# Kernel tuning notes

Hardware: AMD Instinct MI355X
Metric: run time of the kernel (lower is better)

## Reference

```python
import jax, jax.numpy as jnp
import numpy as np

B, N, M, C, K = 2, 8192, 4096, 64, 16
HID = 256
EPS_BN = 1e-5


def setup_inputs() -> dict:
    key = jax.random.key(0)
    ks = jax.random.split(key, 16)
    def rn(i, shape, scale=1.0):
        return jax.random.normal(ks[i], shape, jnp.float32) * scale
    return {
        "pcl": rn(0, (B, M, 3)),
        "pcl_noise": rn(1, (B, N, 3)),
        "feature": rn(2, (B, M, C)),
        # MLP_CONV (2d 1x1): 6 -> 256 (BN+ReLU) -> C
        "w2a": rn(3, (HID, 6), 0.3), "b2a": rn(4, (HID,), 0.1),
        "g2a": 1.0 + rn(5, (HID,), 0.1), "bt2a": rn(6, (HID,), 0.1),
        "w2b": rn(7, (C, HID), 0.1), "b2b": rn(8, (C,), 0.1),
        # MLP_CONV_1d: 3C -> C (BN+ReLU) -> C
        "w1a": rn(9, (C, 3 * C), 0.1), "b1a": rn(10, (C,), 0.1),
        "g1a": 1.0 + rn(11, (C,), 0.1), "bt1a": rn(12, (C,), 0.1),
        "w1b": rn(13, (C, C), 0.1), "b1b": rn(14, (C,), 0.1),
    }


def _sqdist(x, y):  # [B,n,3],[B,m,3] -> [B,n,m]
    return (jnp.sum(x * x, -1, keepdims=True)
            - 2.0 * jnp.einsum('bnc,bmc->bnm', x, y)
            + jnp.sum(y * y, -1)[:, None, :])


def _gather(x, idx):  # x [B,M,D], idx [B,...] -> [B,...,D]
    return jax.vmap(lambda xb, ib: xb[ib])(x, idx)


def _bn(h, g, b):  # inference BatchNorm: running mean 0, var 1
    return h * (g / jnp.sqrt(1.0 + EPS_BN)) + b


def reference(pcl, pcl_noise, feature, w2a, b2a, g2a, bt2a, w2b, b2b,
              w1a, b1a, g1a, bt1a, w1b, b1b):
    # nearest clean point for each noisy point (knn_points K=1)
    close_idx = jnp.argmin(_sqdist(pcl_noise, pcl), axis=-1)          # [B,N]
    close_point = _gather(pcl, close_idx)                             # [B,N,3]
    # K nearest neighbors of close_point within pcl (dil_knn, d=1)
    _, idx = jax.lax.top_k(-_sqdist(close_point, pcl), K)             # [B,N,K]
    knn_points = _gather(pcl, idx)[:, :, 1:, :]                       # [B,N,K-1,3]
    knn_feat = _gather(feature, idx)[:, :, 1:, :]                     # [B,N,K-1,C]
    close_feat = _gather(feature, close_idx)                          # [B,N,C]

    delta = knn_points - pcl_noise[:, :, None, :]                     # [B,N,K-1,3]
    dst = jnp.linalg.norm(delta, axis=-1)                             # [B,N,K-1]
    e = jnp.exp(-10.0 * dst)
    weight = e / (jnp.sum(e, -1, keepdims=True) + 1e-7)               # [B,N,K-1]

    cp = jnp.broadcast_to(close_point[:, :, None, :], delta.shape)
    delta_points = jnp.concatenate([delta, cp], axis=-1)              # [B,N,K-1,6]

    # MLP_CONV2 (1x1 convs over channel dim)
    h = jnp.einsum('bnkc,oc->bnko', delta_points, w2a) + b2a
    h = jax.nn.relu(_bn(h, g2a, bt2a))
    pf = jnp.einsum('bnkc,oc->bnko', h, w2b) + b2b                    # [B,N,K-1,C]

    point_feature = jnp.einsum('bnk,bnkc->bnc', weight, pf)           # [B,N,C]
    co_feature = jnp.einsum('bnk,bnkc->bnc', weight, knn_feat)        # [B,N,C]
    df = jnp.concatenate([close_feat, co_feature, point_feature], -1)  # [B,N,3C]

    # MLP_CONV_1d
    h1 = jnp.einsum('bnc,oc->bno', df, w1a) + b1a
    h1 = jax.nn.relu(_bn(h1, g1a, bt1a))
    return jnp.einsum('bnc,oc->bno', h1, w1b) + b1b                   # [B,N,C]
```

## Files before the change

### kernel.cpp

```cpp
#include <hip/hip_runtime.h>
#include <float.h>

typedef unsigned short u16;
typedef unsigned int u32;
typedef unsigned char u8;

typedef float f32x4 __attribute__((ext_vector_type(4)));
typedef short bh8   __attribute__((ext_vector_type(8)));

__device__ __forceinline__ float bf(u16 u) { return __uint_as_float(((u32)u) << 16); }
__device__ __forceinline__ u16 f2bf(float v) {
    u32 x = __float_as_uint(v);
    u32 r = x + 0x7fffu + ((x >> 16) & 1u);
    return (u16)(r >> 16);
}
__device__ __forceinline__ int detect_f32(const void* probe) {
    const u16* u = (const u16*)probe;
    u16 v = u[(threadIdx.x & 63) * 2];
    int e = (int)((v >> 7) & 0xFF);
    int moderate = (e >= 100) && (e <= 140);
    return __popcll(__ballot(moderate)) < 48;
}
__device__ __forceinline__ float ldv(int f32, const void* p, int i) {
    return f32 ? ((const float*)p)[i] : bf(((const u16*)p)[i]);
}
__device__ __forceinline__ float dot3(float x0, float x1, float x2,
                                      float y0, float y1, float y2) {
    return __fmaf_rn(x2, y2, __fmaf_rn(x1, y1, __fmul_rn(x0, y0)));
}
__device__ __forceinline__ u32 mkey32(float d) {
    u32 f = __float_as_uint(d);
    return f ^ (u32)((((int)f) >> 31) | 0x80000000);
}
__device__ __forceinline__ bh8 ldb(const void* p) { return *(const bh8*)p; }
__device__ __forceinline__ f32x4 mfma16(bh8 a, bh8 b, f32x4 c) {
    return __builtin_amdgcn_mfma_f32_16x16x32_bf16(a, b, c, 0, 0, 0);
}

__global__ __launch_bounds__(256) void k_pre(const void* __restrict__ probe,
                                             const void* __restrict__ w2b,
                                             const void* __restrict__ w1a,
                                             const void* __restrict__ w1b,
                                             u32* __restrict__ canonb,
                                             const void* __restrict__ pcl,
                                             float4* __restrict__ pcl4) {
    int f32 = detect_f32(probe);
    int bx = blockIdx.x, t = threadIdx.x;
    if (bx < 64) {
        int ix = bx * 256 + t;
        const void* src; int j;
        if (ix < 8192)       { src = w2b; j = ix; }
        else if (ix < 14336) { src = w1a; j = ix - 8192; }
        else                 { src = w1b; j = ix - 14336; }
        u32 out;
        if (f32) {
            const float* f = (const float*)src;
            out = ((u32)f2bf(f[2*j+1]) << 16) | (u32)f2bf(f[2*j]);
        } else {
            const u16* su = (const u16*)src;
            out = ((u32)su[2*j+1] << 16) | (u32)su[2*j];
        }
        canonb[ix] = out;
    } else {
        int i = (bx - 64) * 256 + t;
        float x = ldv(f32, pcl, i*3+0), y = ldv(f32, pcl, i*3+1), z = ldv(f32, pcl, i*3+2);
        float s = __fadd_rn(__fadd_rn(__fmul_rn(x,x), __fmul_rn(y,y)), __fmul_rn(z,z));
        pcl4[i] = make_float4(x, y, z, s);
    }
}

__global__ __launch_bounds__(256) void k_close(const float4* __restrict__ pcl4,
                                               const void* __restrict__ noise,
                                               u16* __restrict__ cidx) {
    __shared__ __align__(16) float4 tile[2048];
    int f32 = detect_f32(noise);
    int t = threadIdx.x, g = t >> 4, s = t & 15;
    int q = blockIdx.x * 16 + g;
    int b = q >> 13;
    const float4* src = pcl4 + ((size_t)b << 12);
    float x0 = ldv(f32, noise, q*3+0), x1 = ldv(f32, noise, q*3+1), x2 = ldv(f32, noise, q*3+2);
    float sx = __fadd_rn(__fadd_rn(__fmul_rn(x0,x0), __fmul_rn(x1,x1)), __fmul_rn(x2,x2));
    float bd = FLT_MAX; int bi = 0;
    for (int ch = 0; ch < 2; ++ch) {
        __syncthreads();
#pragma unroll
        for (int i = 0; i < 8; ++i) { int ix = t + (i << 8); tile[ix] = src[(ch << 11) + ix]; }
        __syncthreads();
        for (int j = 0; j < 128; ++j) {
            int cl = (j << 4) + s;
            float4 p = tile[cl];
            float dot = dot3(x0, x1, x2, p.x, p.y, p.z);
            float d = __fadd_rn(__fsub_rn(sx, __fmul_rn(2.0f, dot)), p.w);
            int c = (ch << 11) + cl;
            if (d < bd) { bd = d; bi = c; }
        }
    }
#pragma unroll
    for (int m = 8; m >= 1; m >>= 1) {
        float od = __shfl_xor(bd, m);
        int   oi = __shfl_xor(bi, m);
        if (od < bd || (od == bd && oi < bi)) { bd = od; bi = oi; }
    }
    if (s == 0) cidx[q] = (u16)(bi & 4095);
}

__global__ __launch_bounds__(256) void k_knnh(const float4* __restrict__ pcl4,
                                              u16* __restrict__ knn) {
    __shared__ u8  bins[4096];
    __shared__ u32 hist[256];
    __shared__ u32 skey[256];
    __shared__ u16 sidx[256];
    __shared__ float rmn[4], rmx[4];
    __shared__ u32 scnt;
    __shared__ int ibst;
    int t = threadIdx.x, lane = t & 63, wv = t >> 6;
    int q = blockIdx.x;
    int b = q >> 12;
    const float4* src = pcl4 + ((size_t)b << 12);
    float4 Q = src[q & 4095];
    float x0 = Q.x, x1 = Q.y, x2 = Q.z, sx = Q.w;
    if (t < 256) hist[t] = 0;
    if (t == 0) scnt = 0;
    {
        float4 p = src[t << 4];
        float dot = dot3(x0, x1, x2, p.x, p.y, p.z);
        float d = __fadd_rn(__fsub_rn(sx, __fmul_rn(2.0f, dot)), p.w);
        float mn = d, mx = d;
#pragma unroll
        for (int m = 32; m >= 1; m >>= 1) {
            mn = fminf(mn, __shfl_xor(mn, m));
            mx = fmaxf(mx, __shfl_xor(mx, m));
        }
        if (lane == 0) { rmn[wv] = mn; rmx[wv] = mx; }
    }
    __syncthreads();
    float dmn = fminf(fminf(rmn[0], rmn[1]), fminf(rmn[2], rmn[3]));
    float dmx = fmaxf(fmaxf(rmx[0], rmx[1]), fmaxf(rmx[2], rmx[3]));
    float sc = 1024.0f / fmaxf(dmx - dmn, 1e-20f);
#pragma unroll 4
    for (int j = 0; j < 16; ++j) {
        int cin = (j << 8) + t;
        float4 p = src[cin];
        float dot = dot3(x0, x1, x2, p.x, p.y, p.z);
        float d = __fadd_rn(__fsub_rn(sx, __fmul_rn(2.0f, dot)), p.w);
        float fb = fminf(fmaxf((d - dmn) * sc, 0.0f), 255.0f);
        int bn = (int)fb;
        bins[cin] = (u8)bn;
        if (bn < 255) atomicAdd(&hist[bn], 1u);
    }
    __syncthreads();
    if (t < 64) {
        u32 c0 = hist[4*lane], c1 = hist[4*lane+1];
        u32 c2 = hist[4*lane+2], c3 = hist[4*lane+3];
        u32 loc = c0 + c1 + c2 + c3;
        u32 x = loc;
#pragma unroll
        for (int off = 1; off < 64; off <<= 1) { u32 v = __shfl_up(x, off); if (lane >= off) x += v; }
        u32 excl = x - loc;
        int cand = 999;
        if (excl + c0 >= 16u) cand = 4*lane;
        else if (excl + c0 + c1 >= 16u) cand = 4*lane + 1;
        else if (excl + c0 + c1 + c2 >= 16u) cand = 4*lane + 2;
        else if (excl + loc >= 16u) cand = 4*lane + 3;
#pragma unroll
        for (int m = 32; m >= 1; m >>= 1) cand = min(cand, __shfl_xor(cand, m));
        if (lane == 0) ibst = cand;
    }
    __syncthreads();
    int bstar = ibst;
#pragma unroll
    for (int j = 0; j < 16; ++j) {
        int cin = (j << 8) + t;
        if ((int)bins[cin] <= bstar) {
            u32 pos = atomicAdd(&scnt, 1u);
            if (pos < 256u) {
                float4 p = src[cin];
                float dot = dot3(x0, x1, x2, p.x, p.y, p.z);
                float d = __fadd_rn(__fsub_rn(sx, __fmul_rn(2.0f, dot)), p.w);
                skey[pos] = mkey32(d);
                sidx[pos] = (u16)cin;
            }
        }
    }
    __syncthreads();
    u32 n = scnt;
    if (n <= 256u) {
        for (u32 e = (u32)t; e < n; e += 256u) {
            u32 k = skey[e]; u32 i = (u32)sidx[e];
            int rank = 0;
            for (u32 j = 0; j < n; ++j) {
                u32 kj = skey[j]; u32 ij = (u32)sidx[j];
                rank += (kj < k) || (kj == k && ij < i);
            }
            if (rank < 16) knn[((size_t)q << 4) + rank] = (u16)i;
        }
    } else if (t < 64) {
        u32 k0=~0u,k1=~0u,k2=~0u,k3=~0u,k4=~0u,k5=~0u,k6=~0u,k7=~0u,
            k8=~0u,k9=~0u,k10=~0u,k11=~0u,k12=~0u,k13=~0u,k14=~0u,k15=~0u;
        u32 i0r=0,i1r=0,i2r=0,i3r=0,i4r=0,i5r=0,i6r=0,i7r=0,
            i8r=0,i9r=0,i10r=0,i11r=0,i12r=0,i13r=0,i14r=0,i15r=0;
        for (int j = 0; j < 64; ++j) {
            int cin = (j << 6) + lane;
            float4 p = src[cin];
            float dot = dot3(x0, x1, x2, p.x, p.y, p.z);
            float d = __fadd_rn(__fsub_rn(sx, __fmul_rn(2.0f, dot)), p.w);
            u32 v = mkey32(d); u32 vi = (u32)cin;
            if (v < k15) {
                { u32 c_=(v<k0); u32 nk=c_?v:k0; u32 nv=c_?k0:v; u32 ni=c_?vi:i0r; u32 nj=c_?i0r:vi; k0=nk;i0r=ni;v=nv;vi=nj; }
                { u32 c_=(v<k1); u32 nk=c_?v:k1; u32 nv=c_?k1:v; u32 ni=c_?vi:i1r; u32 nj=c_?i1r:vi; k1=nk;i1r=ni;v=nv;vi=nj; }
                { u32 c_=(v<k2); u32 nk=c_?v:k2; u32 nv=c_?k2:v; u32 ni=c_?vi:i2r; u32 nj=c_?i2r:vi; k2=nk;i2r=ni;v=nv;vi=nj; }
                { u32 c_=(v<k3); u32 nk=c_?v:k3; u32 nv=c_?k3:v; u32 ni=c_?vi:i3r; u32 nj=c_?i3r:vi; k3=nk;i3r=ni;v=nv;vi=nj; }
                { u32 c_=(v<k4); u32 nk=c_?v:k4; u32 nv=c_?k4:v; u32 ni=c_?vi:i4r; u32 nj=c_?i4r:vi; k4=nk;i4r=ni;v=nv;vi=nj; }
                { u32 c_=(v<k5); u32 nk=c_?v:k5; u32 nv=c_?k5:v; u32 ni=c_?vi:i5r; u32 nj=c_?i5r:vi; k5=nk;i5r=ni;v=nv;vi=nj; }
                { u32 c_=(v<k6); u32 nk=c_?v:k6; u32 nv=c_?k6:v; u32 ni=c_?vi:i6r; u32 nj=c_?i6r:vi; k6=nk;i6r=ni;v=nv;vi=nj; }
                { u32 c_=(v<k7); u32 nk=c_?v:k7; u32 nv=c_?k7:v; u32 ni=c_?vi:i7r; u32 nj=c_?i7r:vi; k7=nk;i7r=ni;v=nv;vi=nj; }
                { u32 c_=(v<k8); u32 nk=c_?v:k8; u32 nv=c_?k8:v; u32 ni=c_?vi:i8r; u32 nj=c_?i8r:vi; k8=nk;i8r=ni;v=nv;vi=nj; }
                { u32 c_=(v<k9); u32 nk=c_?v:k9; u32 nv=c_?k9:v; u32 ni=c_?vi:i9r; u32 nj=c_?i9r:vi; k9=nk;i9r=ni;v=nv;vi=nj; }
                { u32 c_=(v<k10); u32 nk=c_?v:k10; u32 nv=c_?k10:v; u32 ni=c_?vi:i10r; u32 nj=c_?i10r:vi; k10=nk;i10r=ni;v=nv;vi=nj; }
                { u32 c_=(v<k11); u32 nk=c_?v:k11; u32 nv=c_?k11:v; u32 ni=c_?vi:i11r; u32 nj=c_?i11r:vi; k11=nk;i11r=ni;v=nv;vi=nj; }
                { u32 c_=(v<k12); u32 nk=c_?v:k12; u32 nv=c_?k12:v; u32 ni=c_?vi:i12r; u32 nj=c_?i12r:vi; k12=nk;i12r=ni;v=nv;vi=nj; }
                { u32 c_=(v<k13); u32 nk=c_?v:k13; u32 nv=c_?k13:v; u32 ni=c_?vi:i13r; u32 nj=c_?i13r:vi; k13=nk;i13r=ni;v=nv;vi=nj; }
                { u32 c_=(v<k14); u32 nk=c_?v:k14; u32 nv=c_?k14:v; u32 ni=c_?vi:i14r; u32 nj=c_?i14r:vi; k14=nk;i14r=ni;v=nv;vi=nj; }
                { u32 c_=(v<k15); u32 nk=c_?v:k15; u32 nv=c_?k15:v; u32 ni=c_?vi:i15r; u32 nj=c_?i15r:vi; k15=nk;i15r=ni;v=nv;vi=nj; }
            }
        }
        u32 myres = 0;
        for (int o = 0; o < 16; ++o) {
            u32 bk = k0, bi2 = i0r;
#pragma unroll
            for (int m = 32; m >= 1; m >>= 1) {
                u32 ok = __shfl_xor(bk, m), oi = __shfl_xor(bi2, m);
                if (ok < bk || (ok == bk && oi < bi2)) { bk = ok; bi2 = oi; }
            }
            if (lane == o) myres = bi2;
            if (k0 == bk && i0r == bi2) {
                k0=k1; i0r=i1r; k1=k2; i1r=i2r; k2=k3; i2r=i3r; k3=k4; i3r=i4r;
                k4=k5; i4r=i5r; k5=k6; i5r=i6r; k6=k7; i6r=i7r; k7=k8; i7r=i8r;
                k8=k9; i8r=i9r; k9=k10; i9r=i10r; k10=k11; i10r=i11r; k11=k12; i11r=i12r;
                k12=k13; i12r=i13r; k13=k14; i13r=i14r; k14=k15; i14r=i15r;
                k15=~0u; i15r=0xFFFFu;
            }
        }
        if (lane < 16) knn[((size_t)q << 4) + lane] = (u16)myres;
    }
}

__global__ __launch_bounds__(256) void k_tail(const float4* __restrict__ pcl4,
                                              const void* __restrict__ noise,
                                              const void* __restrict__ feat,
                                              const u16* __restrict__ cidx,
                                              const u16* __restrict__ knn,
                                              const void* __restrict__ w2a,
                                              const void* __restrict__ b2a,
                                              const void* __restrict__ g2a,
                                              const void* __restrict__ bt2a,
                                              const u32* __restrict__ canonb,
                                              const void* __restrict__ b2b,
                                              const void* __restrict__ b1a,
                                              const void* __restrict__ g1a,
                                              const void* __restrict__ bt1a,
                                              const void* __restrict__ b1b,
                                              void* __restrict__ outp) {
    __shared__ __align__(16) char arena[39744];
    char* dpb_hi = arena;
    char* dpb_lo = arena + 4352;
    char* wbt    = arena + 8704;
    char* wsbp   = arena + 9984;
    u16*  jbuf   = (u16*)(arena + 10048);
    char* hbm_   = arena + 10560;
    char* dfm    = arena + 27200;
    char* h1m    = arena;

    int f32 = detect_f32(noise);
    int t = threadIdx.x, lane = t & 63, wv = t >> 6;
    int g = lane >> 4, l15 = lane & 15;
    int qbb = blockIdx.x * 16;
    int o_lane = wv * 16 + l15;
    const float rbn = 1.0f / sqrtf(1.0f + 1e-5f);
    const char* cb = (const char*)canonb;
    const f32x4 zero4 = {0.f, 0.f, 0.f, 0.f};

    float of2r[4];
    bh8 wH[4];
#pragma unroll
    for (int j = 0; j < 4; ++j) {
        int oh = wv*64 + j*16 + l15;
        float sc = ldv(f32, g2a, oh) * rbn;
        of2r[j] = ldv(f32, b2a, oh) * sc + ldv(f32, bt2a, oh);
        bh8 wz = (bh8){0,0,0,0,0,0,0,0};
        if (g < 3) {
#pragma unroll
            for (int c = 0; c < 6; ++c) {
                float wval = ldv(f32, w2a, oh*6 + c) * sc;
                u16 h = f2bf(wval);
                u16 e = (g == 2) ? f2bf(wval - bf(h)) : h;
                wz[c] = (short)e;
            }
        }
        wH[j] = wz;
    }
    float s1o  = ldv(f32, g1a, o_lane) * rbn;
    float o1o  = ldv(f32, b1a, o_lane) * s1o + ldv(f32, bt1a, o_lane);
    float b2bo = ldv(f32, b2b, o_lane);
    float b1fo = ldv(f32, b1b, o_lane);

    {
        int s = lane & 15;
        int ql = wv*4 + (lane >> 4);
        int q = qbb + ql;
        int b = q >> 13;
        int pbase = b << 12;
        int ci = ((int)cidx[q]) & 4095;
        float4 cp = pcl4[pbase + ci];
        float x0 = ldv(f32, noise, q*3+0), x1 = ldv(f32, noise, q*3+1), x2 = ldv(f32, noise, q*3+2);
        float e = 0.0f;
        if (s >= 1) {
            int jk = ((int)knn[(size_t)(pbase + ci) * 16 + s]) & 4095;
            float4 p = pcl4[pbase + jk];
            float d0 = p.x - x0, d1 = p.y - x1, d2 = p.z - x2;
            float dst = sqrtf(__fadd_rn(__fadd_rn(__fmul_rn(d0,d0), __fmul_rn(d1,d1)), __fmul_rn(d2,d2)));
            e = expf(-10.0f * dst);
            float v6[6] = {d0, d1, d2, cp.x, cp.y, cp.z};
            bh8 HW = (bh8){0,0,0,0,0,0,0,0};
            bh8 LW = (bh8){0,0,0,0,0,0,0,0};
#pragma unroll
            for (int c = 0; c < 6; ++c) {
                u16 hh = f2bf(v6[c]);
                u16 ll = f2bf(v6[c] - bf(hh));
                HW[c] = (short)hh;
                LW[c] = (short)ll;
            }
            *(bh8*)(dpb_hi + (ql*17 + s)*16) = HW;
            *(bh8*)(dpb_lo + (ql*17 + s)*16) = LW;
            jbuf[ql*16 + s] = (u16)jk;
        }
        float es = e;
#pragma unroll
        for (int m = 8; m >= 1; m >>= 1) es += __shfl_xor(es, m, 16);
        float den = es + 1e-7f;
        if (s >= 1) *(float*)(wbt + s*80 + ql*4) = e / den;
        if (s == 0) *(float*)(wsbp + ql*4) = es / den;
    }
    __syncthreads();

#pragma unroll
    for (int qq = 0; qq < 4; ++qq) {
        int qloc = wv*4 + qq;
        int q = qbb + qloc;
        int b = q >> 13;
        int pbase = b << 13;
        pbase = (q >> 13) << 12;
        int ci = ((int)cidx[q]) & 4095;
        size_t fcb = ((size_t)(pbase + ci)) << 6;
        float c0, c1 = 0.0f;
        if (f32) {
            const float* ff = (const float*)feat;
            c0 = ff[fcb + lane];
#pragma unroll
            for (int k = 1; k < 16; ++k) {
                float wk = *(const float*)(wbt + k*80 + qloc*4);
                c1 += wk * ff[(((size_t)(pbase + (int)jbuf[qloc*16 + k])) << 6) + lane];
            }
        } else {
            const u16* fb = (const u16*)feat;
            c0 = bf(fb[fcb + lane]);
#pragma unroll
            for (int k = 1; k < 16; ++k) {
                float wk = *(const float*)(wbt + k*80 + qloc*4);
                c1 += wk * bf(fb[(((size_t)(pbase + (int)jbuf[qloc*16 + k])) << 6) + lane]);
            }
        }
        char* dr = dfm + qloc*784;
        u16 h0 = f2bf(c0); u16 l0 = f2bf(c0 - bf(h0));
        u16 h1v = f2bf(c1); u16 l1v = f2bf(c1 - bf(h1v));
        *(u16*)(dr + (size_t)lane*2)         = h0;
        *(u16*)(dr + (size_t)(192+lane)*2)   = l0;
        *(u16*)(dr + (size_t)(64+lane)*2)    = h1v;
        *(u16*)(dr + (size_t)(256+lane)*2)   = l1v;
    }

    {
        f32x4 hba[4];
#pragma unroll
        for (int j = 0; j < 4; ++j) hba[j] = zero4;
#pragma unroll 2
        for (int k = 1; k < 16; ++k) {
            bh8 af;
            if (g < 3) {
                const char* base = (g == 1) ? dpb_lo : dpb_hi;
                af = ldb(base + (l15*17 + k)*16);
            } else {
                af = (bh8){0,0,0,0,0,0,0,0};
            }
            f32x4 wk4 = *(const f32x4*)(wbt + k*80 + g*16);
#pragma unroll
            for (int j = 0; j < 4; ++j) {
                f32x4 d = mfma16(af, wH[j], zero4);
#pragma unroll
                for (int r = 0; r < 4; ++r)
                    hba[j][r] += wk4[r] * fmaxf(d[r] + of2r[j], 0.0f);
            }
        }
#pragma unroll
        for (int j = 0; j < 4; ++j)
#pragma unroll
            for (int r = 0; r < 4; ++r) {
                int q = g*4 + r;
                int o = wv*64 + j*16 + l15;
                float x = hba[j][r];
                u16 h = f2bf(x); u16 l = f2bf(x - bf(h));
                *(u16*)(hbm_ + q*1040 + (size_t)o*2)       = h;
                *(u16*)(hbm_ + q*1040 + 512 + (size_t)o*2) = l;
            }
    }
    __syncthreads();

    {
        f32x4 acA = zero4, acB = zero4;
#pragma unroll 2
        for (int ks = 0; ks < 8; ++ks) {
            bh8 bw = ldb(cb + (size_t)o_lane*512 + ks*64 + g*16);
            bh8 aH = ldb(hbm_ + l15*1040 + ks*64 + g*16);
            bh8 aL = ldb(hbm_ + l15*1040 + 512 + ks*64 + g*16);
            acA = mfma16(aH, bw, acA);
            acB = mfma16(aL, bw, acB);
        }
        f32x4 wsb4 = *(const f32x4*)(wsbp + g*16);
#pragma unroll
        for (int r = 0; r < 4; ++r) {
            int q = g*4 + r;
            float pf = acA[r] + acB[r] + b2bo * wsb4[r];
            u16 h = f2bf(pf); u16 l = f2bf(pf - bf(h));
            *(u16*)(dfm + q*784 + (size_t)(128 + o_lane)*2) = h;
            *(u16*)(dfm + q*784 + (size_t)(320 + o_lane)*2) = l;
        }
    }
    __syncthreads();

    {
        f32x4 acA = zero4, acB = zero4;
#pragma unroll 2
        for (int ks = 0; ks < 6; ++ks) {
            bh8 bw = ldb(cb + 32768 + (size_t)o_lane*384 + ks*64 + g*16);
            bh8 aH = ldb(dfm + l15*784 + ks*64 + g*16);
            bh8 aL = ldb(dfm + l15*784 + 384 + ks*64 + g*16);
            acA = mfma16(aH, bw, acA);
            acB = mfma16(aL, bw, acB);
        }
#pragma unroll
        for (int r = 0; r < 4; ++r) {
            int q = g*4 + r;
            float z = (acA[r] + acB[r]) * s1o + o1o;
            z = fmaxf(z, 0.0f);
            u16 h = f2bf(z); u16 l = f2bf(z - bf(h));
            *(u16*)(h1m + q*272 + (size_t)o_lane*2)       = h;
            *(u16*)(h1m + q*272 + 128 + (size_t)o_lane*2) = l;
        }
    }
    __syncthreads();

    {
        bh8 bw0 = ldb(cb + 57344 + (size_t)o_lane*128 + g*16);
        bh8 bw1 = ldb(cb + 57344 + (size_t)o_lane*128 + 64 + g*16);
        f32x4 ac = zero4;
        { bh8 a = ldb(h1m + l15*272 +   0 + g*16); ac = mfma16(a, bw0, ac); }
        { bh8 a = ldb(h1m + l15*272 +  64 + g*16); ac = mfma16(a, bw1, ac); }
        { bh8 a = ldb(h1m + l15*272 + 128 + g*16); ac = mfma16(a, bw0, ac); }
        { bh8 a = ldb(h1m + l15*272 + 192 + g*16); ac = mfma16(a, bw1, ac); }
#pragma unroll
        for (int r = 0; r < 4; ++r) {
            int q = g*4 + r;
            float ov = ac[r] + b1fo;
            size_t ob = ((size_t)(qbb + q) << 6) + o_lane;
            if (f32) ((float*)outp)[ob] = ov;
            else     ((u16*)outp)[ob]   = f2bf(ov);
        }
    }
}

extern "C" void kernel_launch(void* const* d_in, const int* in_sizes, int n_in,
                              void* d_out, int out_size, void* d_ws, size_t ws_size,
                              hipStream_t stream) {
    const void* pcl   = d_in[0];
    const void* noise = d_in[1];
    const void* feat  = d_in[2];
    const void* w2a   = d_in[3];
    const void* b2a   = d_in[4];
    const void* g2a   = d_in[5];
    const void* bt2a  = d_in[6];
    const void* w2b   = d_in[7];
    const void* b2b   = d_in[8];
    const void* w1a   = d_in[9];
    const void* b1a   = d_in[10];
    const void* g1a   = d_in[11];
    const void* bt1a  = d_in[12];
    const void* w1b   = d_in[13];
    const void* b1b   = d_in[14];

    char* ws = (char*)d_ws;
    float4* pcl4 = (float4*)ws;
    u16* cidx = (u16*)(ws + 131072);
    u16* knn  = (u16*)(ws + 163840);
    u32* canonb = (u32*)(ws + 425984);

    k_pre  <<<96,   256, 0, stream>>>(noise, w2b, w1a, w1b, canonb, pcl, pcl4);
    k_close<<<1024, 256, 0, stream>>>(pcl4, noise, cidx);
    k_knnh <<<8192, 256, 0, stream>>>(pcl4, knn);
    k_tail <<<1024, 256, 0, stream>>>(pcl4, noise, feat, cidx, knn,
                                      w2a, b2a, g2a, bt2a, canonb, b2b,
                                      b1a, g1a, bt1a, b1b, d_out);
}
```

Measured before the change: 200.4 us.

## Merge nearest-point and KNN kernels into one interleaved launch

Fuses k_close and k_knnh into a single k_sel launch. Block index mod 9 selects the role: one in nine blocks does the nearest-clean-point search and the other eight each do one KNN query, all sharing a 16KB shared arena, so the two independent stages overlap on the GPU and one launch is removed. The close search now uses a smaller 1024-point tile over four chunks to fit the shared arena. In k_tail, the weight and bias setup is moved after the feature gather and that loop is no longer unrolled, which is meant to reduce register pressure. The cost is divergent block roles with unequal work inside one grid.

```diff
diff --git a/kernel.cpp b/kernel.cpp
--- a/kernel.cpp
+++ b/kernel.cpp
@@ -69,58 +69,65 @@
     }
 }
 
-__global__ __launch_bounds__(256) void k_close(const float4* __restrict__ pcl4,
-                                               const void* __restrict__ noise,
-                                               u16* __restrict__ cidx) {
-    __shared__ __align__(16) float4 tile[2048];
-    int f32 = detect_f32(noise);
-    int t = threadIdx.x, g = t >> 4, s = t & 15;
-    int q = blockIdx.x * 16 + g;
-    int b = q >> 13;
-    const float4* src = pcl4 + ((size_t)b << 12);
-    float x0 = ldv(f32, noise, q*3+0), x1 = ldv(f32, noise, q*3+1), x2 = ldv(f32, noise, q*3+2);
-    float sx = __fadd_rn(__fadd_rn(__fmul_rn(x0,x0), __fmul_rn(x1,x1)), __fmul_rn(x2,x2));
-    float bd = FLT_MAX; int bi = 0;
-    for (int ch = 0; ch < 2; ++ch) {
-        __syncthreads();
-#pragma unroll
-        for (int i = 0; i < 8; ++i) { int ix = t + (i << 8); tile[ix] = src[(ch << 11) + ix]; }
-        __syncthreads();
-        for (int j = 0; j < 128; ++j) {
-            int cl = (j << 4) + s;
-            float4 p = tile[cl];
-            float dot = dot3(x0, x1, x2, p.x, p.y, p.z);
-            float d = __fadd_rn(__fsub_rn(sx, __fmul_rn(2.0f, dot)), p.w);
-            int c = (ch << 11) + cl;
-            if (d < bd) { bd = d; bi = c; }
-        }
-    }
-#pragma unroll
-    for (int m = 8; m >= 1; m >>= 1) {
-        float od = __shfl_xor(bd, m);
-        int   oi = __shfl_xor(bi, m);
-        if (od < bd || (od == bd && oi < bi)) { bd = od; bi = oi; }
-    }
-    if (s == 0) cidx[q] = (u16)(bi & 4095);
-}
-
-__global__ __launch_bounds__(256) void k_knnh(const float4* __restrict__ pcl4,
-                                              u16* __restrict__ knn) {
-    __shared__ u8  bins[4096];
-    __shared__ u32 hist[256];
-    __shared__ u32 skey[256];
-    __shared__ u16 sidx[256];
-    __shared__ float rmn[4], rmx[4];
-    __shared__ u32 scnt;
-    __shared__ int ibst;
+__global__ __launch_bounds__(256) void k_sel(const float4* __restrict__ pcl4,
+                                             const void* __restrict__ noise,
+                                             u16* __restrict__ cidx,
+                                             u16* __restrict__ knn) {
+    __shared__ __align__(16) char arena[16384];
+    int bx = blockIdx.x;
+    int r9 = bx % 9, c9 = bx / 9;
     int t = threadIdx.x, lane = t & 63, wv = t >> 6;
-    int q = blockIdx.x;
+
+    if (r9 == 0) {
+        float4* tile = (float4*)arena;
+        int f32 = detect_f32(noise);
+        int g = t >> 4, s = t & 15;
+        int q = c9 * 16 + g;
+        int b = q >> 13;
+        const float4* src = pcl4 + ((size_t)b << 12);
+        float x0 = ldv(f32, noise, q*3+0), x1 = ldv(f32, noise, q*3+1), x2 = ldv(f32, noise, q*3+2);
+        float sx = __fadd_rn(__fadd_rn(__fmul_rn(x0,x0), __fmul_rn(x1,x1)), __fmul_rn(x2,x2));
+        float bd = FLT_MAX; int bi = 0;
+        for (int ch = 0; ch < 4; ++ch) {
+            __syncthreads();
+#pragma unroll
+            for (int i = 0; i < 4; ++i) { int ix = t + (i << 8); tile[ix] = src[(ch << 10) + ix]; }
+            __syncthreads();
+            for (int j = 0; j < 64; ++j) {
+                int cl = (j << 4) + s;
+                float4 p = tile[cl];
+                float dot = dot3(x0, x1, x2, p.x, p.y, p.z);
+                float d = __fadd_rn(__fsub_rn(sx, __fmul_rn(2.0f, dot)), p.w);
+                int c = (ch << 10) + cl;
+                if (d < bd) { bd = d; bi = c; }
+            }
+        }
+#pragma unroll
+        for (int m = 8; m >= 1; m >>= 1) {
+            float od = __shfl_xor(bd, m);
+            int   oi = __shfl_xor(bi, m);
+            if (od < bd || (od == bd && oi < bi)) { bd = od; bi = oi; }
+        }
+        if (s == 0) cidx[q] = (u16)(bi & 4095);
+        return;
+    }
+
+    u8*  bins = (u8*)arena;
+    u32* hist = (u32*)(arena + 4096);
+    u32* skey = (u32*)(arena + 5120);
+    u16* sidx = (u16*)(arena + 6144);
+    float* rmn = (float*)(arena + 6656);
+    float* rmx = (float*)(arena + 6672);
+    u32* scnt = (u32*)(arena + 6688);
+    int* ibst = (int*)(arena + 6692);
+
+    int q = c9 * 8 + (r9 - 1);
     int b = q >> 12;
     const float4* src = pcl4 + ((size_t)b << 12);
     float4 Q = src[q & 4095];
     float x0 = Q.x, x1 = Q.y, x2 = Q.z, sx = Q.w;
-    if (t < 256) hist[t] = 0;
-    if (t == 0) scnt = 0;
+    hist[t] = 0;
+    if (t == 0) *scnt = 0;
     {
         float4 p = src[t << 4];
         float dot = dot3(x0, x1, x2, p.x, p.y, p.z);
@@ -164,15 +171,15 @@
         else if (excl + loc >= 16u) cand = 4*lane + 3;
 #pragma unroll
         for (int m = 32; m >= 1; m >>= 1) cand = min(cand, __shfl_xor(cand, m));
-        if (lane == 0) ibst = cand;
-    }
-    __syncthreads();
-    int bstar = ibst;
+        if (lane == 0) *ibst = cand;
+    }
+    __syncthreads();
+    int bstar = *ibst;
 #pragma unroll
     for (int j = 0; j < 16; ++j) {
         int cin = (j << 8) + t;
         if ((int)bins[cin] <= bstar) {
-            u32 pos = atomicAdd(&scnt, 1u);
+            u32 pos = atomicAdd(scnt, 1u);
             if (pos < 256u) {
                 float4 p = src[cin];
                 float dot = dot3(x0, x1, x2, p.x, p.y, p.z);
@@ -183,7 +190,7 @@
         }
     }
     __syncthreads();
-    u32 n = scnt;
+    u32 n = *scnt;
     if (n <= 256u) {
         for (u32 e = (u32)t; e < n; e += 256u) {
             u32 k = skey[e]; u32 i = (u32)sidx[e];
@@ -280,36 +287,11 @@
     const char* cb = (const char*)canonb;
     const f32x4 zero4 = {0.f, 0.f, 0.f, 0.f};
 
-    float of2r[4];
-    bh8 wH[4];
-#pragma unroll
-    for (int j = 0; j < 4; ++j) {
-        int oh = wv*64 + j*16 + l15;
-        float sc = ldv(f32, g2a, oh) * rbn;
-        of2r[j] = ldv(f32, b2a, oh) * sc + ldv(f32, bt2a, oh);
-        bh8 wz = (bh8){0,0,0,0,0,0,0,0};
-        if (g < 3) {
-#pragma unroll
-            for (int c = 0; c < 6; ++c) {
-                float wval = ldv(f32, w2a, oh*6 + c) * sc;
-                u16 h = f2bf(wval);
-                u16 e = (g == 2) ? f2bf(wval - bf(h)) : h;
-                wz[c] = (short)e;
-            }
-        }
-        wH[j] = wz;
-    }
-    float s1o  = ldv(f32, g1a, o_lane) * rbn;
-    float o1o  = ldv(f32, b1a, o_lane) * s1o + ldv(f32, bt1a, o_lane);
-    float b2bo = ldv(f32, b2b, o_lane);
-    float b1fo = ldv(f32, b1b, o_lane);
-
     {
         int s = lane & 15;
         int ql = wv*4 + (lane >> 4);
         int q = qbb + ql;
-        int b = q >> 13;
-        int pbase = b << 12;
+        int pbase = (q >> 13) << 12;
         int ci = ((int)cidx[q]) & 4095;
         float4 cp = pcl4[pbase + ci];
         float x0 = ldv(f32, noise, q*3+0), x1 = ldv(f32, noise, q*3+1), x2 = ldv(f32, noise, q*3+2);
@@ -343,13 +325,11 @@
     }
     __syncthreads();
 
-#pragma unroll
+#pragma unroll 1
     for (int qq = 0; qq < 4; ++qq) {
         int qloc = wv*4 + qq;
         int q = qbb + qloc;
-        int b = q >> 13;
-        int pbase = b << 13;
-        pbase = (q >> 13) << 12;
+        int pbase = (q >> 13) << 12;
         int ci = ((int)cidx[q]) & 4095;
         size_t fcb = ((size_t)(pbase + ci)) << 6;
         float c0, c1 = 0.0f;
@@ -378,6 +358,30 @@
         *(u16*)(dr + (size_t)(64+lane)*2)    = h1v;
         *(u16*)(dr + (size_t)(256+lane)*2)   = l1v;
     }
+
+    float of2r[4];
+    bh8 wH[4];
+#pragma unroll
+    for (int j = 0; j < 4; ++j) {
+        int oh = wv*64 + j*16 + l15;
+        float sc = ldv(f32, g2a, oh) * rbn;
+        of2r[j] = ldv(f32, b2a, oh) * sc + ldv(f32, bt2a, oh);
+        bh8 wz = (bh8){0,0,0,0,0,0,0,0};
+        if (g < 3) {
+#pragma unroll
+            for (int c = 0; c < 6; ++c) {
+                float wval = ldv(f32, w2a, oh*6 + c) * sc;
+                u16 h = f2bf(wval);
+                u16 e = (g == 2) ? f2bf(wval - bf(h)) : h;
+                wz[c] = (short)e;
+            }
+        }
+        wH[j] = wz;
+    }
+    float s1o  = ldv(f32, g1a, o_lane) * rbn;
+    float o1o  = ldv(f32, b1a, o_lane) * s1o + ldv(f32, bt1a, o_lane);
+    float b2bo = ldv(f32, b2b, o_lane);
+    float b1fo = ldv(f32, b1b, o_lane);
 
     {
         f32x4 hba[4];
@@ -504,8 +508,7 @@
     u32* canonb = (u32*)(ws + 425984);
 
     k_pre  <<<96,   256, 0, stream>>>(noise, w2b, w1a, w1b, canonb, pcl, pcl4);
-    k_close<<<1024, 256, 0, stream>>>(pcl4, noise, cidx);
-    k_knnh <<<8192, 256, 0, stream>>>(pcl4, knn);
+    k_sel  <<<9216, 256, 0, stream>>>(pcl4, noise, cidx, knn);
     k_tail <<<1024, 256, 0, stream>>>(pcl4, noise, feat, cidx, knn,
                                       w2a, b2a, g2a, bt2a, canonb, b2b,
                                       b1a, g1a, bt1a, b1b, d_out);
```

Measured after the change: 211.0 us. +5.3%, slower.
